# Kernel optimization log

Measured on AMD Instinct MI355X. Metric: run time of the kernel, lower is better.

The kernel has to match this reference:

```python
import jax, jax.numpy as jnp
import numpy as np

T = 48  # top-T from init

def setup_inputs() -> dict:
    key = jax.random.key(0)
    ks = jax.random.split(key, 8)
    B, C, H, W = 16, 512, 32, 32
    tc = C // 8
    return {
        "x": jax.random.normal(ks[0], (B, C, H, W), jnp.float32),
        "fW": jax.random.normal(ks[1], (tc, C), jnp.float32) * 0.05,
        "fb": jax.random.normal(ks[2], (tc,), jnp.float32) * 0.05,
        "gW": jax.random.normal(ks[3], (tc, C), jnp.float32) * 0.05,
        "gb": jax.random.normal(ks[4], (tc,), jnp.float32) * 0.05,
        "hW": jax.random.normal(ks[5], (C, C), jnp.float32) * 0.05,
        "hb": jax.random.normal(ks[6], (C,), jnp.float32) * 0.05,
        "scale": jax.random.normal(ks[7], (1,), jnp.float32),
    }

def reference(x, fW, fb, gW, gb, hW, hb, scale):
    B, C, H, W = x.shape
    tc = fW.shape[0]
    HW = H * W
    # normalize by Frobenius norm over (batch, channel) -> [H, W]
    xn = x / jnp.linalg.norm(x, axis=(0, 1))[None, None]  # [B,C,H,W]
    # 1x1 convs, output already channel-last [B,H,W,out]
    f = jnp.einsum('bchw,oc->bhwo', xn, fW) + fb          # [B,H,W,tc]
    g = jnp.einsum('bchw,oc->bhwo', xn, gW) + gb          # [B,H,W,tc]
    h = jnp.einsum('bchw,oc->bhwo', xn, hW) + hb          # [B,H,W,C]
    xp = jnp.transpose(xn, (0, 2, 3, 1))                  # [B,H,W,C]
    # scores: queries H-major, keys W-major (faithful to permute(0,3,2,1).reshape)
    g_keys = jnp.transpose(g, (0, 3, 2, 1)).reshape(B, tc, HW)  # [B,tc,W*H]
    s = jnp.matmul(f.reshape(B, HW, tc), g_keys)          # [B,HW,HW]
    beta = jax.nn.softmax(s, axis=-1)
    o = jnp.matmul(beta, h.reshape(B, HW, C)).reshape(B, H, W, C)
    fdd = scale * o + xp                                  # [B,H,W,C]
    # per-batch correlation: fdd[b] ([H,W,C]) @ fdd[b].reshape(C,HW)
    corr = jnp.einsum('bhwc,bcn->bhwn', fdd, fdd.reshape(B, C, HW))  # [B,H,W,HW]
    top = jax.lax.top_k(corr, T)[0]                       # descending top-T values
    top = jax.nn.relu(top)
    top = top / jnp.linalg.norm(top, axis=(0, 1))[None, None]  # norm over (B,H) -> [W,T]
    return jnp.transpose(top, (0, 3, 1, 2))               # [B,T,H,W]
```

## Files before the change

kernel.cpp:

```cpp
#include <hip/hip_runtime.h>
#include <cstdint>
#include <cstddef>

#define B_   16
#define C_   512
#define H_   32
#define W_   32
#define HW_  1024
#define TC_  64
#define T_   48

typedef unsigned short u16;
typedef __attribute__((ext_vector_type(8))) short short8v;
typedef __attribute__((ext_vector_type(4))) float f32x4;

__device__ __forceinline__ u16 tobf(float x) {
    unsigned u = __float_as_uint(x);
    return (u16)((u + 0x7FFFu + ((u >> 16) & 1u)) >> 16);
}
__device__ __forceinline__ float frombf(u16 h) {
    return __uint_as_float(((unsigned)h) << 16);
}

__device__ __forceinline__ void gld16(const void* g, void* l) {
    __builtin_amdgcn_global_load_lds(
        (const __attribute__((address_space(1))) void*)g,
        (__attribute__((address_space(3))) void*)l, 16, 0, 0);
}

__global__ void k_colsq(const float* __restrict__ x, float* __restrict__ partial) {
    int bid = blockIdx.x;
    int col = (bid & 3) * 256 + threadIdx.x;
    int r0  = (bid >> 2) * 256;
    const float* p = x + (size_t)r0 * HW_ + col;
    float s = 0.f;
    for (int r = 0; r < 256; ++r) { float v = p[(size_t)r * HW_]; s += v * v; }
    partial[(size_t)(bid >> 2) * HW_ + col] = s;
}

__global__ void k_rsqrt(const float* __restrict__ partial, float* __restrict__ ninv) {
    int i = blockIdx.x * 256 + threadIdx.x;
    if (i < HW_) {
        float s = 0.f;
        for (int r = 0; r < 32; ++r) s += partial[(size_t)r * HW_ + i];
        ninv[i] = rsqrtf(s);
    }
}

__global__ void k_transpose(const float* __restrict__ x, const float* __restrict__ ninv,
                            u16* __restrict__ obH) {
    __shared__ float tile[32][33];
    int b  = blockIdx.z;
    int m0 = blockIdx.x * 32, c0 = blockIdx.y * 32;
    int tx = threadIdx.x, ty = threadIdx.y;
    const float* xb = x + (size_t)b * C_ * HW_;
    #pragma unroll
    for (int j = 0; j < 32; j += 8)
        tile[ty + j][tx] = xb[(size_t)(c0 + ty + j) * HW_ + m0 + tx];
    __syncthreads();
    size_t base = (size_t)b * HW_ * C_;
    #pragma unroll
    for (int j = 0; j < 32; j += 8) {
        int m = m0 + ty + j;
        obH[base + (size_t)m * C_ + c0 + tx] = tobf(tile[tx][ty + j] * ninv[m]);
    }
}

__global__ void k_packW(const float* __restrict__ in, u16* __restrict__ oh) {
    size_t i = (size_t)blockIdx.x * 256 + threadIdx.x;
    oh[i] = tobf(in[i]);
}
__global__ void k_packFG(const float* __restrict__ fW, const float* __restrict__ gW,
                         const float* __restrict__ fb, const float* __restrict__ gb,
                         u16* __restrict__ oh, float* __restrict__ fgb) {
    int idx = blockIdx.x * 256 + threadIdx.x;
    int row = idx >> 9, c = idx & 511;
    float v = (row < 64) ? fW[row * 512 + c] : gW[(row - 64) * 512 + c];
    oh[idx] = tobf(v);
    if (idx < 128) fgb[idx] = (idx < 64) ? fb[idx] : gb[idx - 64];
}

template<int PERMB, int EPI>
__global__ __launch_bounds__(256) void k_gemm1(
    const u16* __restrict__ A, const u16* __restrict__ Bm,
    const float* __restrict__ bias,
    float* __restrict__ Cf, u16* __restrict__ Ch,
    const float* __restrict__ scaleP,
    int N, int K, int lda, int ldb, long sA, long sB, long sC)
{
    __shared__ u16 lds[2 * 8192];
    const int b = blockIdx.z;
    const u16* pA = A + (size_t)b * sA;
    const u16* pB = Bm + (size_t)b * sB;
    const int m0 = blockIdx.y * 128, n0 = blockIdx.x * 128;
    const int tid = threadIdx.x, wave = tid >> 6, lane = tid & 63;
    const int wm = wave >> 1, wn = wave & 1;
    const int g = lane >> 4;

    f32x4 acc[4][4];
    #pragma unroll
    for (int i = 0; i < 4; ++i)
        #pragma unroll
        for (int j = 0; j < 4; ++j) { f32x4 z = {0.f,0.f,0.f,0.f}; acc[i][j] = z; }

    auto STAGE = [&](int kt, int half) {
        const int k0 = kt << 5;
        u16* lb = lds + half * 8192;
        #pragma unroll
        for (int q = 0; q < 4; ++q) {
            int ci = wave * 4 + q;
            bool isA = ci < 8;
            int li = ci & 7;
            const u16* gp = isA ? pA : pB;
            int ld = isA ? lda : ldb;
            int rb = isA ? m0 : n0;
            int rp = li * 8 + (lane >> 3);
            int gg = (lane & 7) ^ (rp & 7);
            int r  = rp * 2 + (gg >> 2);
            int kc = k0 + (gg & 3) * 8;
            int rowg = rb + r;
            if (PERMB && !isA) rowg = ((rowg & 31) << 5) | (rowg >> 5);
            gld16(gp + (size_t)rowg * ld + kc,
                  lb + (isA ? 0 : 4096) + li * 512 + lane * 8);
        }
    };
    auto COMPUTE = [&](int half) {
        const u16* As = lds + half * 8192;
        const u16* Bs = As + 4096;
        short8v av[4];
        #pragma unroll
        for (int i = 0; i < 4; ++i) {
            int r = wm * 64 + i * 16 + (lane & 15);
            int rp = r >> 1, gg = ((r & 1) << 2) + g;
            av[i] = *(const short8v*)(As + rp * 64 + ((gg ^ (rp & 7)) << 3));
        }
        #pragma unroll
        for (int j = 0; j < 4; ++j) {
            int r = wn * 64 + j * 16 + (lane & 15);
            int rp = r >> 1, gg = ((r & 1) << 2) + g;
            short8v bv = *(const short8v*)(Bs + rp * 64 + ((gg ^ (rp & 7)) << 3));
            #pragma unroll
            for (int i = 0; i < 4; ++i)
                acc[i][j] = __builtin_amdgcn_mfma_f32_16x16x32_bf16(av[i], bv, acc[i][j], 0, 0, 0);
        }
    };

    const int nkt = K >> 5;
    STAGE(0, 0);
    int cur = 0;
    for (int kt = 0; kt < nkt; ++kt) {
        if (kt + 1 < nkt) {
            STAGE(kt + 1, cur ^ 1);
            asm volatile("s_waitcnt vmcnt(4)" ::: "memory");
        } else {
            asm volatile("s_waitcnt vmcnt(0)" ::: "memory");
        }
        __builtin_amdgcn_s_barrier();
        __builtin_amdgcn_sched_barrier(0);
        COMPUTE(cur);
        __builtin_amdgcn_sched_barrier(0);
        __builtin_amdgcn_s_barrier();
        cur ^= 1;
    }

    const float sc = (EPI == 2) ? scaleP[0] : 0.f;
    const int colbase = n0 + wn * 64 + (lane & 15);
    const int rowbase = m0 + wm * 64 + ((lane >> 4) << 2);
    #pragma unroll
    for (int i = 0; i < 4; ++i)
        #pragma unroll
        for (int j = 0; j < 4; ++j) {
            int col = colbase + j * 16;
            #pragma unroll
            for (int rg = 0; rg < 4; ++rg) {
                int row = rowbase + i * 16 + rg;
                size_t idx = (size_t)b * sC + (size_t)row * N + col;
                float a = acc[i][j][rg];
                if (EPI == 0)      Cf[idx] = a;
                else if (EPI == 2) Ch[idx] = tobf(sc * a + frombf(Ch[idx]));
                else if (EPI == 4) Ch[idx] = tobf(a);
                else if (EPI == 5) Ch[idx] = tobf(a + bias[row]);
                else               Ch[idx] = tobf(a + bias[col]);
            }
        }
}

template<int PERMB, int EPI>
__global__ __launch_bounds__(512) void k_gemm2(
    const u16* __restrict__ A, const u16* __restrict__ Bm,
    const float* __restrict__ bias,
    float* __restrict__ Cf, u16* __restrict__ Ch,
    const float* __restrict__ scaleP,
    int N, int K, int lda, int ldb, long sA, long sB, long sC)
{
    __shared__ u16 lds[2 * 12288];
    const int b = blockIdx.z;
    const u16* pA = A + (size_t)b * sA;
    const u16* pB = Bm + (size_t)b * sB;
    const int m0 = blockIdx.y * 128, n0 = blockIdx.x * 256;
    const int tid = threadIdx.x, wave = tid >> 6, lane = tid & 63;
    const int wm = wave >> 2, wn = wave & 3;
    const int g = lane >> 4;

    f32x4 acc[4][4];
    #pragma unroll
    for (int i = 0; i < 4; ++i)
        #pragma unroll
        for (int j = 0; j < 4; ++j) { f32x4 z = {0.f,0.f,0.f,0.f}; acc[i][j] = z; }

    auto STAGE = [&](int kt, int half) {
        const int k0 = kt << 5;
        u16* lb = lds + half * 12288;
        #pragma unroll
        for (int q = 0; q < 3; ++q) {
            int ci = wave * 3 + q;
            bool isA = ci < 8;
            int li = isA ? ci : ci - 8;
            const u16* gp = isA ? pA : pB;
            int ld = isA ? lda : ldb;
            int rb = isA ? m0 : n0;
            int rp = li * 8 + (lane >> 3);
            int gg = (lane & 7) ^ (rp & 7);
            int r  = rp * 2 + (gg >> 2);
            int kc = k0 + (gg & 3) * 8;
            int rowg = rb + r;
            if (PERMB && !isA) rowg = ((rowg & 31) << 5) | (rowg >> 5);
            gld16(gp + (size_t)rowg * ld + kc,
                  lb + (isA ? 0 : 4096) + li * 512 + lane * 8);
        }
    };
    auto COMPUTE = [&](int half) {
        const u16* As = lds + half * 12288;
        const u16* Bs = As + 4096;
        short8v av[4];
        #pragma unroll
        for (int i = 0; i < 4; ++i) {
            int r = wm * 64 + i * 16 + (lane & 15);
            int rp = r >> 1, gg = ((r & 1) << 2) + g;
            av[i] = *(const short8v*)(As + rp * 64 + ((gg ^ (rp & 7)) << 3));
        }
        #pragma unroll
        for (int j = 0; j < 4; ++j) {
            int r = wn * 64 + j * 16 + (lane & 15);
            int rp = r >> 1, gg = ((r & 1) << 2) + g;
            short8v bv = *(const short8v*)(Bs + rp * 64 + ((gg ^ (rp & 7)) << 3));
            #pragma unroll
            for (int i = 0; i < 4; ++i)
                acc[i][j] = __builtin_amdgcn_mfma_f32_16x16x32_bf16(av[i], bv, acc[i][j], 0, 0, 0);
        }
    };

    const int nkt = K >> 5;
    STAGE(0, 0);
    int cur = 0;
    for (int kt = 0; kt < nkt; ++kt) {
        if (kt + 1 < nkt) {
            STAGE(kt + 1, cur ^ 1);
            asm volatile("s_waitcnt vmcnt(3)" ::: "memory");
        } else {
            asm volatile("s_waitcnt vmcnt(0)" ::: "memory");
        }
        __builtin_amdgcn_s_barrier();
        __builtin_amdgcn_sched_barrier(0);
        COMPUTE(cur);
        __builtin_amdgcn_sched_barrier(0);
        __builtin_amdgcn_s_barrier();
        cur ^= 1;
    }

    const float sc = (EPI == 2) ? scaleP[0] : 0.f;
    const int colbase = n0 + wn * 64 + (lane & 15);
    const int rowbase = m0 + wm * 64 + ((lane >> 4) << 2);
    #pragma unroll
    for (int i = 0; i < 4; ++i)
        #pragma unroll
        for (int j = 0; j < 4; ++j) {
            int col = colbase + j * 16;
            #pragma unroll
            for (int rg = 0; rg < 4; ++rg) {
                int row = rowbase + i * 16 + rg;
                size_t idx = (size_t)b * sC + (size_t)row * N + col;
                float a = acc[i][j][rg];
                if (EPI == 0)      Cf[idx] = a;
                else if (EPI == 2) Ch[idx] = tobf(sc * a + frombf(Ch[idx]));
                else if (EPI == 4) Ch[idx] = tobf(a);
                else if (EPI == 5) Ch[idx] = tobf(a + bias[row]);
                else               Ch[idx] = tobf(a + bias[col]);
            }
        }
}

__global__ __launch_bounds__(256) void k_softmax(u16* __restrict__ S) {
    size_t row = blockIdx.x;
    u16* r = S + row * (size_t)HW_;
    int t = threadIdx.x;
    ushort4 raw = ((const ushort4*)r)[t];
    float v0 = frombf(raw.x), v1 = frombf(raw.y), v2 = frombf(raw.z), v3 = frombf(raw.w);

    __shared__ float redm[4], reds[4];
    int wid = t >> 6, lane = t & 63;

    float m = fmaxf(fmaxf(v0, v1), fmaxf(v2, v3));
    for (int o = 32; o > 0; o >>= 1) m = fmaxf(m, __shfl_down(m, o));
    if (lane == 0) redm[wid] = m;
    __syncthreads();
    if (t == 0) redm[0] = fmaxf(fmaxf(redm[0], redm[1]), fmaxf(redm[2], redm[3]));
    __syncthreads();
    m = redm[0];

    v0 = expf(v0 - m); v1 = expf(v1 - m); v2 = expf(v2 - m); v3 = expf(v3 - m);
    float s = v0 + v1 + v2 + v3;
    for (int o = 32; o > 0; o >>= 1) s += __shfl_down(s, o);
    if (lane == 0) reds[wid] = s;
    __syncthreads();
    if (t == 0) reds[0] = reds[0] + reds[1] + reds[2] + reds[3];
    __syncthreads();
    float inv = 1.f / reds[0];
    ushort4 o4;
    o4.x = tobf(v0 * inv); o4.y = tobf(v1 * inv);
    o4.z = tobf(v2 * inv); o4.w = tobf(v3 * inv);
    ((ushort4*)r)[t] = o4;
}

__global__ void k_tposeU1(const u16* __restrict__ src, u16* __restrict__ dst) {
    __shared__ u16 tile[32][33];
    int b = blockIdx.z;
    const u16* sb = src + (size_t)b * (C_ * HW_);
    u16* db = dst + (size_t)b * (C_ * HW_);
    int c0 = blockIdx.x * 32, r0 = blockIdx.y * 32;
    int tx = threadIdx.x, ty = threadIdx.y;
    #pragma unroll
    for (int j = 0; j < 32; j += 8)
        tile[ty + j][tx] = sb[(size_t)(r0 + ty + j) * HW_ + c0 + tx];
    __syncthreads();
    #pragma unroll
    for (int j = 0; j < 32; j += 8)
        db[(size_t)(c0 + ty + j) * C_ + r0 + tx] = tile[tx][ty + j];
}

__device__ __forceinline__ float sort64_desc(float v, int lane) {
    #pragma unroll
    for (int k = 2; k <= 64; k <<= 1) {
        #pragma unroll
        for (int j = k >> 1; j > 0; j >>= 1) {
            float o = __shfl_xor(v, j);
            bool takeMax = (((lane & k) == 0) == ((lane & j) == 0));
            v = takeMax ? fmaxf(v, o) : fminf(v, o);
        }
    }
    return v;
}
__device__ __forceinline__ float bmerge64_desc(float a, float b, int lane) {
    float br = __shfl(b, 63 - lane);
    float c = fmaxf(a, br);
    #pragma unroll
    for (int j = 32; j > 0; j >>= 1) {
        float o = __shfl_xor(c, j);
        c = ((lane & j) == 0) ? fmaxf(c, o) : fminf(c, o);
    }
    return c;
}

__global__ __launch_bounds__(256) void k_topk(const float* __restrict__ corr,
                                              float* __restrict__ topv) {
    __shared__ float buf[4][1024];
    int wave = threadIdx.x >> 6, lane = threadIdx.x & 63;
    int row = blockIdx.x * 4 + wave;
    const float4* rp = (const float4*)(corr + (size_t)row * HW_);

    float4 e[4];
    #pragma unroll
    for (int q = 0; q < 4; ++q) e[q] = rp[lane * 4 + q];

    float gm = -INFINITY;
    #pragma unroll
    for (int q = 0; q < 4; ++q)
        gm = fmaxf(gm, fmaxf(fmaxf(e[q].x, e[q].y), fmaxf(e[q].z, e[q].w)));
    float sorted = sort64_desc(gm, lane);
    float tau = __shfl(sorted, T_ - 1);

    int c = 0;
    #pragma unroll
    for (int q = 0; q < 4; ++q)
        c += (e[q].x >= tau) + (e[q].y >= tau) + (e[q].z >= tau) + (e[q].w >= tau);
    int sc = c;
    #pragma unroll
    for (int o = 1; o < 64; o <<= 1) {
        int t2 = __shfl_up(sc, o);
        if (lane >= o) sc += t2;
    }
    int off = sc - c;
    int cnt = __shfl(sc, 63);

    float* wb = buf[wave];
    #pragma unroll
    for (int q = 0; q < 4; ++q) {
        if (e[q].x >= tau) wb[off++] = e[q].x;
        if (e[q].y >= tau) wb[off++] = e[q].y;
        if (e[q].z >= tau) wb[off++] = e[q].z;
        if (e[q].w >= tau) wb[off++] = e[q].w;
    }

    float* orow = topv + (size_t)row * T_;
    if (cnt <= 64) {
        float a = (lane < cnt) ? wb[lane] : -INFINITY;
        a = sort64_desc(a, lane);
        if (lane < T_) orow[lane] = fmaxf(a, 0.f);
    } else if (cnt <= 128) {
        float a  = sort64_desc(wb[lane], lane);
        float b2 = sort64_desc((lane < cnt - 64) ? wb[64 + lane] : -INFINITY, lane);
        float m2 = bmerge64_desc(a, b2, lane);
        if (lane < T_) orow[lane] = fmaxf(m2, 0.f);
    } else {
        int P = 256; while (P < cnt) P <<= 1;
        for (int i = cnt + lane; i < P; i += 64) wb[i] = -INFINITY;
        for (int k = 2; k <= P; k <<= 1)
            for (int j = k >> 1; j > 0; j >>= 1)
                for (int t2 = lane; t2 < P; t2 += 64) {
                    int ixj = t2 ^ j;
                    if (ixj > t2) {
                        float a = wb[t2], b3 = wb[ixj];
                        bool desc = ((t2 & k) == 0);
                        if (desc ? (a < b3) : (a > b3)) { wb[t2] = b3; wb[ixj] = a; }
                    }
                }
        if (lane < T_) orow[lane] = fmaxf(wb[lane], 0.f);
    }
}

__global__ void k_colss(const float* __restrict__ topv, float* __restrict__ colss) {
    int o = blockIdx.x;
    int w = o / T_, t = o % T_;
    int lane = threadIdx.x;
    float s = 0.f;
    for (int i = lane; i < 512; i += 64) {
        int b = i >> 5, h = i & 31;
        float v = topv[(size_t)((b << 10) + (h << 5) + w) * T_ + t];
        s += v * v;
    }
    for (int off = 32; off > 0; off >>= 1) s += __shfl_down(s, off);
    if (lane == 0) colss[o] = s;
}

__global__ void k_final(const float* __restrict__ topv, const float* __restrict__ colss,
                        float* __restrict__ out) {
    int idx = blockIdx.x * 256 + threadIdx.x;
    if (idx >= B_ * T_ * HW_) return;
    int w = idx & 31;
    int h = (idx >> 5) & 31;
    int t = (idx >> 10) % T_;
    int b = idx / (T_ * HW_);
    float v = topv[(size_t)((b << 10) + (h << 5) + w) * T_ + t];
    out[idx] = v * rsqrtf(colss[w * T_ + t]);
}

extern "C" void kernel_launch(void* const* d_in, const int* in_sizes, int n_in,
                              void* d_out, int out_size, void* d_ws, size_t ws_size,
                              hipStream_t stream) {
    const float* x     = (const float*)d_in[0];
    const float* fW    = (const float*)d_in[1];
    const float* fb    = (const float*)d_in[2];
    const float* gW    = (const float*)d_in[3];
    const float* gb    = (const float*)d_in[4];
    const float* hW    = (const float*)d_in[5];
    const float* hb    = (const float*)d_in[6];
    const float* scale = (const float*)d_in[7];
    float* out = (float*)d_out;

    char* wsb = (char*)d_ws;
    float* part = (float*)(wsb + 0);
    float* ninv = (float*)(wsb + 131072);
    u16*   hWh  = (u16*)(wsb + 135168);
    u16*   fgWh = (u16*)(wsb + 1183744);
    float* fgb  = (float*)(wsb + 1445888);
    u16*   xnH  = (u16*)(wsb + 1446400);
    u16*   fgH  = (u16*)(wsb + 35000832);
    u16*   fgL  = (u16*)(wsb + 39195136);
    u16*   hvTH = (u16*)(wsb + 43389440);
    float* S    = (float*)(wsb + 76943872);
    float* topv = (float*)fgH;
    float* colss= (float*)fgL;
    u16*   Sp   = (u16*)S;

    const long sXn = 524288;
    const long sFG = 131072;
    const long sS  = 1048576;

    k_colsq<<<128, 256, 0, stream>>>(x, part);
    k_rsqrt<<<4, 256, 0, stream>>>(part, ninv);

    k_transpose<<<dim3(32, 16, 16), dim3(32, 8), 0, stream>>>(x, ninv, xnH);

    k_packW<<<1024, 256, 0, stream>>>(hW, hWh);
    k_packFG<<<256, 256, 0, stream>>>(fW, gW, fb, gb, fgWh, fgb);

    k_gemm1<0, 6><<<dim3(1, 8, 16), 256, 0, stream>>>(
        xnH, fgWh, fgb, nullptr, fgH, nullptr,
        128, 512, 512, 512, sXn, 0, sFG);

    k_gemm2<0, 5><<<dim3(4, 4, 16), 512, 0, stream>>>(
        hWh, xnH, hb, nullptr, hvTH, nullptr,
        1024, 512, 512, 512, 0, sXn, sXn);

    k_gemm2<1, 4><<<dim3(4, 8, 16), 512, 0, stream>>>(
        fgH, fgH + 64, nullptr, nullptr, Sp, nullptr,
        1024, 64, 128, 128, sFG, sFG, sS);

    k_softmax<<<B_ * HW_, 256, 0, stream>>>(Sp);

    k_gemm2<0, 2><<<dim3(2, 8, 16), 512, 0, stream>>>(
        Sp, hvTH, nullptr, nullptr, xnH, scale,
        512, 1024, 1024, 1024, sS, sXn, sXn);

    k_tposeU1<<<dim3(32, 16, 16), dim3(32, 8), 0, stream>>>(xnH, hvTH);

    k_gemm2<0, 0><<<dim3(4, 8, 16), 512, 0, stream>>>(
        xnH, hvTH, nullptr, S, nullptr, nullptr,
        1024, 512, 512, 512, sXn, sXn, sS);

    k_topk<<<B_ * HW_ / 4, 256, 0, stream>>>(S, topv);

    k_colss<<<W_ * T_, 64, 0, stream>>>(topv, colss);
    k_final<<<(B_ * T_ * HW_ + 255) / 256, 256, 0, stream>>>(topv, colss, out);
}
```

Baseline: 213.8 us.

## Triple-buffer GEMM LDS pipeline, use 128x128 tiles, split column-norm reduction finer

Both GEMM kernels move from double to triple LDS buffering and prefetch two k-tiles ahead, with adjusted vmcnt waits, so global loads overlap more of the compute. Three large GEMMs switch from the 128x256 512-thread kernel to the 128x128 256-thread kernel, doubling the grid. The column sum-of-squares reduction uses twice as many blocks with shorter loops. The workspace offsets are compacted. Tripled LDS per block may lower occupancy.

```diff
diff --git a/kernel.cpp b/kernel.cpp
--- a/kernel.cpp
+++ b/kernel.cpp
@@ -31,10 +31,10 @@
 __global__ void k_colsq(const float* __restrict__ x, float* __restrict__ partial) {
     int bid = blockIdx.x;
     int col = (bid & 3) * 256 + threadIdx.x;
-    int r0  = (bid >> 2) * 256;
+    int r0  = (bid >> 2) * 128;
     const float* p = x + (size_t)r0 * HW_ + col;
     float s = 0.f;
-    for (int r = 0; r < 256; ++r) { float v = p[(size_t)r * HW_]; s += v * v; }
+    for (int r = 0; r < 128; ++r) { float v = p[(size_t)r * HW_]; s += v * v; }
     partial[(size_t)(bid >> 2) * HW_ + col] = s;
 }
 
@@ -42,7 +42,7 @@
     int i = blockIdx.x * 256 + threadIdx.x;
     if (i < HW_) {
         float s = 0.f;
-        for (int r = 0; r < 32; ++r) s += partial[(size_t)r * HW_ + i];
+        for (int r = 0; r < 64; ++r) s += partial[(size_t)r * HW_ + i];
         ninv[i] = rsqrtf(s);
     }
 }
@@ -88,7 +88,7 @@
     const float* __restrict__ scaleP,
     int N, int K, int lda, int ldb, long sA, long sB, long sC)
 {
-    __shared__ u16 lds[2 * 8192];
+    __shared__ u16 lds[3 * 8192];
     const int b = blockIdx.z;
     const u16* pA = A + (size_t)b * sA;
     const u16* pB = Bm + (size_t)b * sB;
@@ -103,9 +103,9 @@
         #pragma unroll
         for (int j = 0; j < 4; ++j) { f32x4 z = {0.f,0.f,0.f,0.f}; acc[i][j] = z; }
 
-    auto STAGE = [&](int kt, int half) {
+    auto STAGE = [&](int kt, int buf) {
         const int k0 = kt << 5;
-        u16* lb = lds + half * 8192;
+        u16* lb = lds + buf * 8192;
         #pragma unroll
         for (int q = 0; q < 4; ++q) {
             int ci = wave * 4 + q;
@@ -124,8 +124,8 @@
                   lb + (isA ? 0 : 4096) + li * 512 + lane * 8);
         }
     };
-    auto COMPUTE = [&](int half) {
-        const u16* As = lds + half * 8192;
+    auto COMPUTE = [&](int buf) {
+        const u16* As = lds + buf * 8192;
         const u16* Bs = As + 4096;
         short8v av[4];
         #pragma unroll
@@ -147,10 +147,14 @@
 
     const int nkt = K >> 5;
     STAGE(0, 0);
+    STAGE(1, 1);
     int cur = 0;
     for (int kt = 0; kt < nkt; ++kt) {
-        if (kt + 1 < nkt) {
-            STAGE(kt + 1, cur ^ 1);
+        int nxt2 = cur + 2; if (nxt2 >= 3) nxt2 -= 3;
+        if (kt + 2 < nkt) {
+            STAGE(kt + 2, nxt2);
+            asm volatile("s_waitcnt vmcnt(8)" ::: "memory");
+        } else if (kt + 1 < nkt) {
             asm volatile("s_waitcnt vmcnt(4)" ::: "memory");
         } else {
             asm volatile("s_waitcnt vmcnt(0)" ::: "memory");
@@ -160,7 +164,7 @@
         COMPUTE(cur);
         __builtin_amdgcn_sched_barrier(0);
         __builtin_amdgcn_s_barrier();
-        cur ^= 1;
+        ++cur; if (cur >= 3) cur -= 3;
     }
 
     const float sc = (EPI == 2) ? scaleP[0] : 0.f;
@@ -193,7 +197,7 @@
     const float* __restrict__ scaleP,
     int N, int K, int lda, int ldb, long sA, long sB, long sC)
 {
-    __shared__ u16 lds[2 * 12288];
+    __shared__ u16 lds[3 * 12288];
     const int b = blockIdx.z;
     const u16* pA = A + (size_t)b * sA;
     const u16* pB = Bm + (size_t)b * sB;
@@ -208,9 +212,9 @@
         #pragma unroll
         for (int j = 0; j < 4; ++j) { f32x4 z = {0.f,0.f,0.f,0.f}; acc[i][j] = z; }
 
-    auto STAGE = [&](int kt, int half) {
+    auto STAGE = [&](int kt, int buf) {
         const int k0 = kt << 5;
-        u16* lb = lds + half * 12288;
+        u16* lb = lds + buf * 12288;
         #pragma unroll
         for (int q = 0; q < 3; ++q) {
             int ci = wave * 3 + q;
@@ -229,8 +233,8 @@
                   lb + (isA ? 0 : 4096) + li * 512 + lane * 8);
         }
     };
-    auto COMPUTE = [&](int half) {
-        const u16* As = lds + half * 12288;
+    auto COMPUTE = [&](int buf) {
+        const u16* As = lds + buf * 12288;
         const u16* Bs = As + 4096;
         short8v av[4];
         #pragma unroll
@@ -252,10 +256,14 @@
 
     const int nkt = K >> 5;
     STAGE(0, 0);
+    STAGE(1, 1);
     int cur = 0;
     for (int kt = 0; kt < nkt; ++kt) {
-        if (kt + 1 < nkt) {
-            STAGE(kt + 1, cur ^ 1);
+        int nxt2 = cur + 2; if (nxt2 >= 3) nxt2 -= 3;
+        if (kt + 2 < nkt) {
+            STAGE(kt + 2, nxt2);
+            asm volatile("s_waitcnt vmcnt(6)" ::: "memory");
+        } else if (kt + 1 < nkt) {
             asm volatile("s_waitcnt vmcnt(3)" ::: "memory");
         } else {
             asm volatile("s_waitcnt vmcnt(0)" ::: "memory");
@@ -265,7 +273,7 @@
         COMPUTE(cur);
         __builtin_amdgcn_sched_barrier(0);
         __builtin_amdgcn_s_barrier();
-        cur ^= 1;
+        ++cur; if (cur >= 3) cur -= 3;
     }
 
     const float sc = (EPI == 2) ? scaleP[0] : 0.f;
@@ -469,15 +477,15 @@
 
     char* wsb = (char*)d_ws;
     float* part = (float*)(wsb + 0);
-    float* ninv = (float*)(wsb + 131072);
-    u16*   hWh  = (u16*)(wsb + 135168);
-    u16*   fgWh = (u16*)(wsb + 1183744);
-    float* fgb  = (float*)(wsb + 1445888);
-    u16*   xnH  = (u16*)(wsb + 1446400);
-    u16*   fgH  = (u16*)(wsb + 35000832);
-    u16*   fgL  = (u16*)(wsb + 39195136);
-    u16*   hvTH = (u16*)(wsb + 43389440);
-    float* S    = (float*)(wsb + 76943872);
+    float* ninv = (float*)(wsb + 262144);
+    u16*   hWh  = (u16*)(wsb + 266240);
+    u16*   fgWh = (u16*)(wsb + 790528);
+    float* fgb  = (float*)(wsb + 921600);
+    u16*   xnH  = (u16*)(wsb + 922112);
+    u16*   fgH  = (u16*)(wsb + 17699328);
+    u16*   fgL  = (u16*)(wsb + 21893632);
+    u16*   hvTH = (u16*)(wsb + 26087936);
+    float* S    = (float*)(wsb + 42865152);
     float* topv = (float*)fgH;
     float* colss= (float*)fgL;
     u16*   Sp   = (u16*)S;
@@ -486,7 +494,7 @@
     const long sFG = 131072;
     const long sS  = 1048576;
 
-    k_colsq<<<128, 256, 0, stream>>>(x, part);
+    k_colsq<<<256, 256, 0, stream>>>(x, part);
     k_rsqrt<<<4, 256, 0, stream>>>(part, ninv);
 
     k_transpose<<<dim3(32, 16, 16), dim3(32, 8), 0, stream>>>(x, ninv, xnH);
@@ -498,7 +506,7 @@
         xnH, fgWh, fgb, nullptr, fgH, nullptr,
         128, 512, 512, 512, sXn, 0, sFG);
 
-    k_gemm2<0, 5><<<dim3(4, 4, 16), 512, 0, stream>>>(
+    k_gemm1<0, 5><<<dim3(8, 4, 16), 256, 0, stream>>>(
         hWh, xnH, hb, nullptr, hvTH, nullptr,
         1024, 512, 512, 512, 0, sXn, sXn);
 
@@ -508,13 +516,13 @@
 
     k_softmax<<<B_ * HW_, 256, 0, stream>>>(Sp);
 
-    k_gemm2<0, 2><<<dim3(2, 8, 16), 512, 0, stream>>>(
+    k_gemm1<0, 2><<<dim3(4, 8, 16), 256, 0, stream>>>(
         Sp, hvTH, nullptr, nullptr, xnH, scale,
         512, 1024, 1024, 1024, sS, sXn, sXn);
 
     k_tposeU1<<<dim3(32, 16, 16), dim3(32, 8), 0, stream>>>(xnH, hvTH);
 
-    k_gemm2<0, 0><<<dim3(4, 8, 16), 512, 0, stream>>>(
+    k_gemm1<0, 0><<<dim3(8, 8, 16), 256, 0, stream>>>(
         xnH, hvTH, nullptr, S, nullptr, nullptr,
         1024, 512, 512, 512, sXn, sXn, sS);
 
```

Result: no change. 215.4 us (+0.8%).
